# Kernel optimization log

Hardware: AMD Instinct MI355X
Metric: run time of the kernel (lower is better)

The kernel has to match this reference:

```python
import jax, jax.numpy as jnp
import numpy as np

B, Q, V, T = 96, 96, 197, 77   # image batch, text batch, visual tokens, text tokens
DV, DT, E = 768, 768, 512      # visual_size, textual_size, embed_size


def l2norm(x):
    # F.normalize(t, dim=-1, p=2) with eps=1e-12
    n = jnp.linalg.norm(x, axis=-1, keepdims=True)
    return x / jnp.maximum(n, 1e-12)


def setup_inputs() -> dict:
    key = jax.random.key(0)
    ks = jax.random.split(key, 12)
    sv = 1.0 / np.sqrt(DV).astype(np.float32)
    st = 1.0 / np.sqrt(DT).astype(np.float32)
    return {
        "visual_cls": jax.random.normal(ks[0], (B, DV), jnp.float32),
        "visual_tokens": jax.random.normal(ks[1], (B, V, DV), jnp.float32),
        "textual_cls": jax.random.normal(ks[2], (Q, DT), jnp.float32),
        "textual_tokens": jax.random.normal(ks[3], (Q, T, DT), jnp.float32),
        "Wv_cls": jax.random.normal(ks[4], (E, DV), jnp.float32) * sv,
        "bv_cls": jnp.zeros((E,), jnp.float32),
        "Wt_cls": jax.random.normal(ks[5], (E, DT), jnp.float32) * st,
        "bt_cls": jnp.zeros((E,), jnp.float32),
        "Wv_tok": jax.random.normal(ks[6], (E, DV), jnp.float32) * sv,
        "bv_tok": jnp.zeros((E,), jnp.float32),
        "Wt_tok": jax.random.normal(ks[7], (E, DT), jnp.float32) * st,
        "bt_tok": jnp.zeros((E,), jnp.float32),
        "text_length": jax.random.randint(ks[8], (Q,), 5, T + 1, jnp.int32),
    }


def reference(visual_cls, visual_tokens, textual_cls, textual_tokens,
              Wv_cls, bv_cls, Wt_cls, bt_cls,
              Wv_tok, bv_tok, Wt_tok, bt_tok, text_length):
    # Linear projections (torch nn.Linear: y = x @ W.T + b)
    v_cls = visual_cls @ Wv_cls.T + bv_cls            # [b, e]
    t_cls = textual_cls @ Wt_cls.T + bt_cls           # [q, e]
    v_tok = l2norm(jnp.einsum('bvd,ed->bve', visual_tokens, Wv_tok) + bv_tok)   # [b, v, e]
    t_tok = l2norm(jnp.einsum('qtd,ed->qte', textual_tokens, Wt_tok) + bt_tok)  # [q, t, e]

    # valid-token mask from caption lengths: mask[q, t]
    mask = (jnp.arange(T)[None, :] < text_length[:, None]).astype(v_tok.dtype)

    # fine-grained token similarity: [b, q, v, t], masked on text tokens
    logits = jnp.einsum('bve,qte->bqvt', v_tok, t_tok) * mask[None, :, None, :]

    text_sum = mask.sum(-1)                           # [q]
    t2v = logits.max(axis=2).sum(axis=2) / text_sum[None, :]   # [b, q]
    v2t = logits.max(axis=3).sum(axis=2) / V                   # [b, q]
    return (v_cls, t_cls, t2v, v2t)
```

## Files before the change

### kernel.cpp

```cpp
#include <hip/hip_runtime.h>

#define NB 96
#define NQ 96
#define NV 197
#define NT 77
#define DK 768
#define DE 512

typedef __attribute__((ext_vector_type(8))) short s16x8;
typedef __attribute__((ext_vector_type(4))) float f32x4;

__device__ __forceinline__ unsigned short f2bf(float f) {
  union { float f; unsigned int u; } v; v.f = f;
  unsigned int u = v.u;
  unsigned int r = u + 0x7fffu + ((u >> 16) & 1u);
  return (unsigned short)(r >> 16);
}

__device__ __forceinline__ unsigned int pack2bf(float a, float b) {
  return (unsigned int)f2bf(a) | ((unsigned int)f2bf(b) << 16);
}

#define GL16(gp, lp, off)                                                \
  __builtin_amdgcn_global_load_lds(                                      \
      (const __attribute__((address_space(1))) void*)(gp),               \
      (__attribute__((address_space(3))) void*)(lp), 16, (off), 0)

#define VM_DRAIN() asm volatile("s_waitcnt vmcnt(0) lgkmcnt(0)" ::: "memory")

__global__ __launch_bounds__(256) void prep_kernel(
    const float* __restrict__ Wv_tok, unsigned short* __restrict__ Wvb,
    const float* __restrict__ Wt_tok, unsigned short* __restrict__ Wtb,
    const float* __restrict__ visual_cls, const float* __restrict__ Wv_cls,
    const float* __restrict__ bv_cls, float* __restrict__ v_cls_o,
    const float* __restrict__ textual_cls, const float* __restrict__ Wt_cls,
    const float* __restrict__ bt_cls, float* __restrict__ t_cls_o) {
  __shared__ float xs[DK];
  const int blk = blockIdx.x;
  const int tid = threadIdx.x;

  if (blk < 768) {
    const float* src = (blk < 384) ? Wv_tok : Wt_tok;
    unsigned short* dst = (blk < 384) ? Wvb : Wtb;
    int i = ((blk < 384) ? blk : (blk - 384)) * 256 + tid;
    float4 x = ((const float4*)src)[i];
    ushort4 h;
    h.x = f2bf(x.x); h.y = f2bf(x.y); h.z = f2bf(x.z); h.w = f2bf(x.w);
    ((ushort4*)dst)[i] = h;
    return;
  }
  const int is_t = (blk >= 864);
  const int row = blk - (is_t ? 864 : 768);
  const float* X = is_t ? textual_cls : visual_cls;
  const float* W = is_t ? Wt_cls : Wv_cls;
  const float* bias = is_t ? bt_cls : bv_cls;
  float* out = is_t ? t_cls_o : v_cls_o;

  const float* xr = X + (long)row * DK;
  for (int i = tid; i < DK; i += 256) xs[i] = xr[i];
  __syncthreads();
  for (int c = tid; c < DE; c += 256) {
    const float* wr = W + (long)c * DK;
    float s = 0.f;
    #pragma unroll 4
    for (int k = 0; k < DK; k += 4) {
      float4 w4 = *(const float4*)(wr + k);
      s += xs[k] * w4.x + xs[k + 1] * w4.y + xs[k + 2] * w4.z + xs[k + 3] * w4.w;
    }
    out[(long)row * DE + c] = s + bias[c];
  }
}

__global__ __launch_bounds__(256, 2) void proj_norm_kernel(
    const float* __restrict__ Xv, const unsigned short* __restrict__ Wvb,
    const float* __restrict__ bv, unsigned short* __restrict__ Yv,
    const float* __restrict__ Xt, const unsigned short* __restrict__ Wtb,
    const float* __restrict__ bt, unsigned short* __restrict__ Yt) {
  __shared__ __align__(16) unsigned short Ws[512 * 64];
  __shared__ __align__(16) unsigned short Xs[64 * 64];
  __shared__ float ssq_lds[4][64];

  const int blk = blockIdx.x;
  const int is_t = (blk >= 296);
  const float* X = is_t ? Xt : Xv;
  const unsigned short* Wb = is_t ? Wtb : Wvb;
  const float* bias = is_t ? bt : bv;
  unsigned short* Y = is_t ? Yt : Yv;
  const int M = is_t ? (NQ * NT) : (NB * NV);
  const long row0 = (long)(is_t ? (blk - 296) : blk) * 64;

  const int tid = threadIdx.x;
  const int wave = tid >> 6;
  const int lane = tid & 63;
  const int l15 = lane & 15;
  const int quad = lane >> 4;

  const int sub = lane >> 3;
  const int swz = ((lane & 7) ^ sub) << 3;
  const unsigned short* pw_base = Wb + (long)(wave * 8 + sub) * DK + swz;

  const int xrow_a = tid >> 3;
  const int xrow_b = xrow_a + 32;
  const int xs8 = tid & 7;
  long gra = row0 + xrow_a; if (gra > M - 1) gra = M - 1;
  long grb = row0 + xrow_b; if (grb > M - 1) grb = M - 1;
  const float* px_a = X + gra * DK + xs8 * 8;
  const float* px_b = X + grb * DK + xs8 * 8;
  const int xaddr_a = (xrow_a << 6) + ((xs8 ^ (xrow_a & 7)) << 3);
  const int xaddr_b = (xrow_b << 6) + ((xs8 ^ (xrow_b & 7)) << 3);

  f32x4 acc[4][8];
  #pragma unroll
  for (int m = 0; m < 4; ++m)
    #pragma unroll
    for (int n = 0; n < 8; ++n)
      acc[m][n] = (f32x4){0.f, 0.f, 0.f, 0.f};

  for (int kc = 0; kc < DK; kc += 64) {
    __syncthreads();
    {
      float4 x0 = *(const float4*)(px_a);
      float4 x1 = *(const float4*)(px_a + 4);
      uint4 h;
      h.x = pack2bf(x0.x, x0.y); h.y = pack2bf(x0.z, x0.w);
      h.z = pack2bf(x1.x, x1.y); h.w = pack2bf(x1.z, x1.w);
      *(uint4*)(&Xs[xaddr_a]) = h;
      x0 = *(const float4*)(px_b);
      x1 = *(const float4*)(px_b + 4);
      h.x = pack2bf(x0.x, x0.y); h.y = pack2bf(x0.z, x0.w);
      h.z = pack2bf(x1.x, x1.y); h.w = pack2bf(x1.z, x1.w);
      *(uint4*)(&Xs[xaddr_b]) = h;
      px_a += 64; px_b += 64;
    }
    {
      const unsigned short* pw = pw_base;
      #pragma unroll
      for (int j = 0; j < 16; ++j) {
        GL16(pw, &Ws[(j * 4 + wave) << 9], 0);
        pw += 32 * DK;
      }
      pw_base += 64;
    }
    VM_DRAIN();
    __syncthreads();
    #pragma unroll
    for (int ks = 0; ks < 2; ++ks) {
      s16x8 af[4];
      #pragma unroll
      for (int mi = 0; mi < 4; ++mi) {
        int arow = mi * 16 + l15;
        af[mi] = *(const s16x8*)&Xs[(arow << 6) + ((((ks << 2) + quad) ^ (arow & 7)) << 3)];
      }
      #pragma unroll
      for (int nt = 0; nt < 8; ++nt) {
        int wrow = wave * 128 + nt * 16 + l15;
        s16x8 bfr = *(const s16x8*)&Ws[(wrow << 6) + ((((ks << 2) + quad) ^ (wrow & 7)) << 3)];
        #pragma unroll
        for (int mi = 0; mi < 4; ++mi)
          acc[mi][nt] = __builtin_amdgcn_mfma_f32_16x16x32_bf16(af[mi], bfr, acc[mi][nt], 0, 0, 0);
      }
    }
  }

  #pragma unroll
  for (int nt = 0; nt < 8; ++nt) {
    float bc = bias[wave * 128 + nt * 16 + l15];
    #pragma unroll
    for (int mi = 0; mi < 4; ++mi) {
      acc[mi][nt].x += bc; acc[mi][nt].y += bc; acc[mi][nt].z += bc; acc[mi][nt].w += bc;
    }
  }

  #pragma unroll
  for (int mi = 0; mi < 4; ++mi)
    #pragma unroll
    for (int r = 0; r < 4; ++r) {
      float t = 0.f;
      #pragma unroll
      for (int nt = 0; nt < 8; ++nt) { float v = acc[mi][nt][r]; t += v * v; }
      t += __shfl_xor(t, 1);
      t += __shfl_xor(t, 2);
      t += __shfl_xor(t, 4);
      t += __shfl_xor(t, 8);
      if (l15 == 0) ssq_lds[wave][mi * 16 + quad * 4 + r] = t;
    }
  __syncthreads();

  #pragma unroll
  for (int mi = 0; mi < 4; ++mi) {
    #pragma unroll
    for (int r = 0; r < 4; ++r) {
      int rr = mi * 16 + quad * 4 + r;
      float tot = ssq_lds[0][rr] + ssq_lds[1][rr] + ssq_lds[2][rr] + ssq_lds[3][rr];
      float scale = (tot > 0.f) ? (1.f / fmaxf(sqrtf(tot), 1e-12f)) : 0.f;
      long grow = row0 + rr;
      if (grow < M) {
        #pragma unroll
        for (int nt = 0; nt < 8; ++nt) {
          int col = wave * 128 + nt * 16 + l15;
          Y[grow * DE + col] = f2bf(acc[mi][nt][r] * scale);
        }
      }
    }
  }
}

__global__ __launch_bounds__(256, 2) void score_kernel(
    const unsigned short* __restrict__ Yv, const unsigned short* __restrict__ Yt,
    const int* __restrict__ tlen, float* __restrict__ t2v, float* __restrict__ v2t) {
  __shared__ __align__(16) unsigned short As[2][104 * 64];
  __shared__ __align__(16) unsigned short Bs[2][80 * 64];
  __shared__ float colbuf[4][160];
  __shared__ float rowsum_lds[4][2];

  const int tid = threadIdx.x;
  const int wave = tid >> 6;
  const int lane = tid & 63;
  const int l15 = lane & 15;
  const int quad = lane >> 4;

  const int idx = blockIdx.x;
  const int span = idx / 384;
  const int r0 = idx - span * 384;
  const int b = span * 8 + (r0 & 7);
  const int qi = r0 >> 3;
  const int q0 = qi * 2;

  const unsigned short* Ab = Yv + (long)b * (NV * DE);
  const unsigned short* Bb = Yt + (long)q0 * (NT * DE);

  {
    unsigned int* za = (unsigned int*)&As[0][0];
    for (int i = tid; i < 6656; i += 256) za[i] = 0;
    unsigned int* zb = (unsigned int*)&Bs[0][0];
    for (int i = tid; i < 5120; i += 256) zb[i] = 0;
  }
  __syncthreads();

  const int ul = lane >> 3;
  const int slot = lane & 7;
  const int kseg = ((slot >> 1) ^ (ul & 3)) << 3;

  auto a_ptr = [&](int s) -> const unsigned short* {
    int row = (s * 8 + ul) * 2 + (slot & 1);
    if (row > NV - 1) row = NV - 1;
    return Ab + row * DE + kseg;
  };
  auto b_ptr = [&](int s) -> const unsigned short* {
    int r = (s * 8 + ul) * 2 + (slot & 1);
    int half = (r >= 80) ? 1 : 0;
    int t = r - 80 * half;
    if (t > NT - 1) t = NT - 1;
    return Bb + (long)half * (NT * DE) + t * DE + kseg;
  };

  const unsigned short* sp0 = a_ptr(wave);
  const unsigned short* sp1 = a_ptr(wave + 4);
  const unsigned short* sp2 = a_ptr(wave + 8);
  const int s3 = (wave == 1) ? 8 : (wave == 2) ? 9 : 12;
  const int b3_is_b = (wave == 1 || wave == 2);
  const unsigned short* sp3 = b3_is_b ? b_ptr(s3) : a_ptr(12);
  const unsigned short* sp4 = b_ptr(wave);
  const unsigned short* sp5 = b_ptr(wave + 4);
  unsigned short* b3p0 = b3_is_b ? &Bs[0][s3 << 9] : &As[0][12 << 9];
  unsigned short* b3p1 = b3_is_b ? &Bs[1][s3 << 9] : &As[1][12 << 9];

  int aoff[4], boff[10];
  #pragma unroll
  for (int i = 0; i < 4; ++i) {
    int arow = (wave + i * 4) * 16 + l15;
    int u = arow >> 1;
    aoff[i] = (u << 6) + (((quad ^ (u & 3)) << 4)) + ((arow & 1) << 3);
  }
  #pragma unroll
  for (int nt = 0; nt < 10; ++nt) {
    int brow = nt * 16 + l15;
    int u = brow >> 1;
    boff[nt] = (u << 6) + (((quad ^ (u & 3)) << 4)) + ((brow & 1) << 3);
  }

  f32x4 acc[4][10];
  #pragma unroll
  for (int i = 0; i < 4; ++i)
    #pragma unroll
    for (int nt = 0; nt < 10; ++nt)
      acc[i][nt] = (f32x4){0.f, 0.f, 0.f, 0.f};

  auto do_compute = [&](int p) {
    s16x8 bf[10];
    #pragma unroll
    for (int nt = 0; nt < 10; ++nt)
      bf[nt] = *(const s16x8*)&Bs[p][boff[nt]];
    #pragma unroll
    for (int i = 0; i < 4; ++i) {
      int mt = wave + (i << 2);
      if (mt < 13) {
        s16x8 af = *(const s16x8*)&As[p][aoff[i]];
        #pragma unroll
        for (int nt = 0; nt < 10; ++nt)
          acc[i][nt] = __builtin_amdgcn_mfma_f32_16x16x32_bf16(af, bf[nt], acc[i][nt], 0, 0, 0);
      }
    }
  };

#define SCORE_STAGE(p)                                                   \
  {                                                                      \
    GL16(sp0, &As[p][(wave) << 9], 0);                                   \
    GL16(sp1, &As[p][(wave + 4) << 9], 0);                               \
    GL16(sp2, &As[p][(wave + 8) << 9], 0);                               \
    GL16(sp3, (p) ? b3p1 : b3p0, 0);                                     \
    GL16(sp4, &Bs[p][(wave) << 9], 0);                                   \
    GL16(sp5, &Bs[p][(wave + 4) << 9], 0);                               \
    sp0 += 32; sp1 += 32; sp2 += 32; sp3 += 32; sp4 += 32; sp5 += 32;    \
  }

#define SCORE_ITER(cur, is_last)                                         \
  {                                                                      \
    VM_DRAIN();                                                          \
    __syncthreads();                                                     \
    if (!(is_last)) SCORE_STAGE(1 - (cur));                              \
    do_compute(cur);                                                     \
  }

  SCORE_STAGE(0)
  SCORE_ITER(0, 0)
  SCORE_ITER(1, 0)
  SCORE_ITER(0, 0)
  SCORE_ITER(1, 0)
  SCORE_ITER(0, 0)
  SCORE_ITER(1, 0)
  SCORE_ITER(0, 0)
  SCORE_ITER(1, 0)
  SCORE_ITER(0, 0)
  SCORE_ITER(1, 0)
  SCORE_ITER(0, 0)
  SCORE_ITER(1, 0)
  SCORE_ITER(0, 0)
  SCORE_ITER(1, 0)
  SCORE_ITER(0, 0)
  SCORE_ITER(1, 1)

#undef SCORE_ITER
#undef SCORE_STAGE

  const int len0 = tlen[q0];
  const int len1 = tlen[q0 + 1];

  #pragma unroll
  for (int nt = 0; nt < 10; ++nt) {
    float m = -1e30f;
    #pragma unroll
    for (int i = 0; i < 4; ++i) {
      int mt = wave + (i << 2);
      if (mt < 13) {
        int mbase = mt * 16 + quad * 4;
        #pragma unroll
        for (int r = 0; r < 4; ++r)
          if (mbase + r < NV) m = fmaxf(m, acc[i][nt][r]);
      }
    }
    m = fmaxf(m, __shfl_xor(m, 16));
    m = fmaxf(m, __shfl_xor(m, 32));
    if (lane < 16) colbuf[wave][nt * 16 + l15] = m;
  }

  float psum[2] = {0.f, 0.f};
  #pragma unroll
  for (int h = 0; h < 2; ++h) {
    int len = h ? len1 : len0;
    #pragma unroll
    for (int i = 0; i < 4; ++i) {
      int mt = wave + (i << 2);
      if (mt < 13) {
        int mbase = mt * 16 + quad * 4;
        #pragma unroll
        for (int r = 0; r < 4; ++r) {
          float rm = -1e30f;
          #pragma unroll
          for (int nt = 0; nt < 5; ++nt) {
            int c = nt * 16 + l15;
            if (c < len) rm = fmaxf(rm, acc[i][h * 5 + nt][r]);
          }
          rm = fmaxf(rm, __shfl_xor(rm, 1));
          rm = fmaxf(rm, __shfl_xor(rm, 2));
          rm = fmaxf(rm, __shfl_xor(rm, 4));
          rm = fmaxf(rm, __shfl_xor(rm, 8));
          if (len < NT) rm = fmaxf(rm, 0.f);
          if (l15 == 0 && (mbase + r) < NV) psum[h] += rm;
        }
      }
    }
    psum[h] += __shfl_xor(psum[h], 16);
    psum[h] += __shfl_xor(psum[h], 32);
  }
  if (lane == 0) { rowsum_lds[wave][0] = psum[0]; rowsum_lds[wave][1] = psum[1]; }
  __syncthreads();

  if (wave < 2) {
    int q = q0 + wave;
    int len = wave ? len1 : len0;
    int cbase = wave * 80;
    float ssum = 0.f;
    for (int c = lane; c < 80; c += 64) {
      if (c < len) {
        float m = fmaxf(fmaxf(colbuf[0][cbase + c], colbuf[1][cbase + c]),
                        fmaxf(colbuf[2][cbase + c], colbuf[3][cbase + c]));
        ssum += m;
      }
    }
    ssum += __shfl_xor(ssum, 1);
    ssum += __shfl_xor(ssum, 2);
    ssum += __shfl_xor(ssum, 4);
    ssum += __shfl_xor(ssum, 8);
    ssum += __shfl_xor(ssum, 16);
    ssum += __shfl_xor(ssum, 32);
    if (lane == 0) {
      float rs = rowsum_lds[0][wave] + rowsum_lds[1][wave] +
                 rowsum_lds[2][wave] + rowsum_lds[3][wave];
      t2v[b * NQ + q] = ssum / (float)len;
      v2t[b * NQ + q] = rs / (float)NV;
    }
  }
}

extern "C" void kernel_launch(void* const* d_in, const int* in_sizes, int n_in,
                              void* d_out, int out_size, void* d_ws, size_t ws_size,
                              hipStream_t stream) {
  (void)in_sizes; (void)n_in; (void)out_size; (void)ws_size;
  const float* visual_cls     = (const float*)d_in[0];
  const float* visual_tokens  = (const float*)d_in[1];
  const float* textual_cls    = (const float*)d_in[2];
  const float* textual_tokens = (const float*)d_in[3];
  const float* Wv_cls = (const float*)d_in[4];
  const float* bv_cls = (const float*)d_in[5];
  const float* Wt_cls = (const float*)d_in[6];
  const float* bt_cls = (const float*)d_in[7];
  const float* Wv_tok = (const float*)d_in[8];
  const float* bv_tok = (const float*)d_in[9];
  const float* Wt_tok = (const float*)d_in[10];
  const float* bt_tok = (const float*)d_in[11];
  const int* text_length = (const int*)d_in[12];

  float* out = (float*)d_out;
  float* v_cls_o = out;
  float* t_cls_o = out + 49152;
  float* t2v_o   = out + 98304;
  float* v2t_o   = out + 107520;

  char* ws = (char*)d_ws;
  unsigned short* Wvb = (unsigned short*)(ws);
  unsigned short* Wtb = (unsigned short*)(ws + 786432);
  unsigned short* Yv  = (unsigned short*)(ws + 1572864);
  unsigned short* Yt  = (unsigned short*)(ws + 20938752);

  prep_kernel<<<960, 256, 0, stream>>>(
      Wv_tok, Wvb, Wt_tok, Wtb,
      visual_cls, Wv_cls, bv_cls, v_cls_o,
      textual_cls, Wt_cls, bt_cls, t_cls_o);

  proj_norm_kernel<<<412, 256, 0, stream>>>(
      visual_tokens, Wvb, bv_tok, Yv,
      textual_tokens, Wtb, bt_tok, Yt);

  score_kernel<<<(NB * NQ) / 2, 256, 0, stream>>>(Yv, Yt, text_length, t2v_o, v2t_o);
}
```

Before: 451.5 us.

## Triple-buffer score kernel K-loop, raise MFMA priority, and remap block order

The score kernel's shared-memory staging goes from two buffers to three, so two K-stages are in flight. Each iteration now waits with a partial vmcnt(6) instead of draining all loads, which lets global-to-LDS copies overlap with MFMA compute. MFMA sections are wrapped in s_setprio to favour compute issue, and the block-to-(b,q) mapping is reordered to change L2 reuse of text and visual tiles. The extra LDS (about 50KB per block) may hurt residency at the launch bound of two blocks per CU.

After: 447.0 us. About the same (-1.0%).

```diff
diff --git a/kernel.cpp b/kernel.cpp
--- a/kernel.cpp
+++ b/kernel.cpp
@@ -208,8 +208,8 @@
 __global__ __launch_bounds__(256, 2) void score_kernel(
     const unsigned short* __restrict__ Yv, const unsigned short* __restrict__ Yt,
     const int* __restrict__ tlen, float* __restrict__ t2v, float* __restrict__ v2t) {
-  __shared__ __align__(16) unsigned short As[2][104 * 64];
-  __shared__ __align__(16) unsigned short Bs[2][80 * 64];
+  __shared__ __align__(16) unsigned short As[3][104 * 64];
+  __shared__ __align__(16) unsigned short Bs[3][80 * 64];
   __shared__ float colbuf[4][160];
   __shared__ float rowsum_lds[4][2];
 
@@ -220,10 +220,11 @@
   const int quad = lane >> 4;
 
   const int idx = blockIdx.x;
-  const int span = idx / 384;
-  const int r0 = idx - span * 384;
-  const int b = span * 8 + (r0 & 7);
-  const int qi = r0 >> 3;
+  const int x = idx & 7;
+  const int g = idx >> 3;
+  const int qi = g / 12;
+  const int bslot = g - qi * 12;
+  const int b = bslot * 8 + x;
   const int q0 = qi * 2;
 
   const unsigned short* Ab = Yv + (long)b * (NV * DE);
@@ -231,9 +232,9 @@
 
   {
     unsigned int* za = (unsigned int*)&As[0][0];
-    for (int i = tid; i < 6656; i += 256) za[i] = 0;
+    for (int i = tid; i < 9984; i += 256) za[i] = 0;
     unsigned int* zb = (unsigned int*)&Bs[0][0];
-    for (int i = tid; i < 5120; i += 256) zb[i] = 0;
+    for (int i = tid; i < 7680; i += 256) zb[i] = 0;
   }
   __syncthreads();
 
@@ -262,8 +263,9 @@
   const unsigned short* sp3 = b3_is_b ? b_ptr(s3) : a_ptr(12);
   const unsigned short* sp4 = b_ptr(wave);
   const unsigned short* sp5 = b_ptr(wave + 4);
-  unsigned short* b3p0 = b3_is_b ? &Bs[0][s3 << 9] : &As[0][12 << 9];
-  unsigned short* b3p1 = b3_is_b ? &Bs[1][s3 << 9] : &As[1][12 << 9];
+  unsigned short* b3d0 = b3_is_b ? &Bs[0][s3 << 9] : &As[0][12 << 9];
+  unsigned short* b3d1 = b3_is_b ? &Bs[1][s3 << 9] : &As[1][12 << 9];
+  unsigned short* b3d2 = b3_is_b ? &Bs[2][s3 << 9] : &As[2][12 << 9];
 
   int aoff[4], boff[10];
   #pragma unroll
@@ -291,6 +293,7 @@
     #pragma unroll
     for (int nt = 0; nt < 10; ++nt)
       bf[nt] = *(const s16x8*)&Bs[p][boff[nt]];
+    __builtin_amdgcn_s_setprio(1);
     #pragma unroll
     for (int i = 0; i < 4; ++i) {
       int mt = wave + (i << 2);
@@ -301,44 +304,46 @@
           acc[i][nt] = __builtin_amdgcn_mfma_f32_16x16x32_bf16(af, bf[nt], acc[i][nt], 0, 0, 0);
       }
     }
+    __builtin_amdgcn_s_setprio(0);
   };
 
-#define SCORE_STAGE(p)                                                   \
+#define SCORE_STAGE(p, b3p)                                              \
   {                                                                      \
     GL16(sp0, &As[p][(wave) << 9], 0);                                   \
     GL16(sp1, &As[p][(wave + 4) << 9], 0);                               \
     GL16(sp2, &As[p][(wave + 8) << 9], 0);                               \
-    GL16(sp3, (p) ? b3p1 : b3p0, 0);                                     \
+    GL16(sp3, (b3p), 0);                                                 \
     GL16(sp4, &Bs[p][(wave) << 9], 0);                                   \
     GL16(sp5, &Bs[p][(wave + 4) << 9], 0);                               \
     sp0 += 32; sp1 += 32; sp2 += 32; sp3 += 32; sp4 += 32; sp5 += 32;    \
   }
 
-#define SCORE_ITER(cur, is_last)                                         \
+#define SCORE_ITER(cur, nxt, b3p, do_stage, WN)                          \
   {                                                                      \
-    VM_DRAIN();                                                          \
+    asm volatile("s_waitcnt vmcnt(" #WN ")" ::: "memory");               \
     __syncthreads();                                                     \
-    if (!(is_last)) SCORE_STAGE(1 - (cur));                              \
+    if (do_stage) SCORE_STAGE(nxt, b3p);                                 \
     do_compute(cur);                                                     \
   }
 
-  SCORE_STAGE(0)
-  SCORE_ITER(0, 0)
-  SCORE_ITER(1, 0)
-  SCORE_ITER(0, 0)
-  SCORE_ITER(1, 0)
-  SCORE_ITER(0, 0)
-  SCORE_ITER(1, 0)
-  SCORE_ITER(0, 0)
-  SCORE_ITER(1, 0)
-  SCORE_ITER(0, 0)
-  SCORE_ITER(1, 0)
-  SCORE_ITER(0, 0)
-  SCORE_ITER(1, 0)
-  SCORE_ITER(0, 0)
-  SCORE_ITER(1, 0)
-  SCORE_ITER(0, 0)
-  SCORE_ITER(1, 1)
+  SCORE_STAGE(0, b3d0)
+  SCORE_STAGE(1, b3d1)
+  SCORE_ITER(0, 2, b3d2, 1, 6)
+  SCORE_ITER(1, 0, b3d0, 1, 6)
+  SCORE_ITER(2, 1, b3d1, 1, 6)
+  SCORE_ITER(0, 2, b3d2, 1, 6)
+  SCORE_ITER(1, 0, b3d0, 1, 6)
+  SCORE_ITER(2, 1, b3d1, 1, 6)
+  SCORE_ITER(0, 2, b3d2, 1, 6)
+  SCORE_ITER(1, 0, b3d0, 1, 6)
+  SCORE_ITER(2, 1, b3d1, 1, 6)
+  SCORE_ITER(0, 2, b3d2, 1, 6)
+  SCORE_ITER(1, 0, b3d0, 1, 6)
+  SCORE_ITER(2, 1, b3d1, 1, 6)
+  SCORE_ITER(0, 2, b3d2, 1, 6)
+  SCORE_ITER(1, 0, b3d0, 1, 6)
+  SCORE_ITER(2, 1, b3d1, 0, 6)
+  SCORE_ITER(0, 2, b3d2, 0, 0)
 
 #undef SCORE_ITER
 #undef SCORE_STAGE
```
